# Optimization experiments

Hardware: AMD Instinct MI355X
Metric: run time of the kernel (lower is better)

The kernel has to match this reference:

```python
import jax, jax.numpy as jnp
import numpy as np


def _grouped_attn(q, k, v, mask, scale):
    # q: [T,H,D], k/v: [S,KH,D], mask: [T,S] or [KH,T,S] (True = visible)
    T, H, D = q.shape
    S, KH, _ = k.shape
    G = H // KH
    qg = q.reshape(T, KH, G, D)
    logits = jnp.einsum('tkgd,skd->kgts', qg, k) * scale
    if mask.ndim == 2:
        mask = jnp.broadcast_to(mask[None], (KH, T, S))
    logits = jnp.where(mask[:, None], logits, -1e30)
    p = jax.nn.softmax(logits, axis=-1)
    valid = mask.any(-1)  # [KH,T]: queries with at least one visible key
    p = jnp.where(valid[:, None, :, None], p, 0.0)
    o = jnp.einsum('kgts,skd->tkgd', p, v).reshape(T, H, D)
    return o, p


def setup_inputs() -> dict:
    key = jax.random.key(0)
    ks = jax.random.split(key, 4)
    T, H, KH, D = 2048, 16, 2, 128
    q = jax.random.normal(ks[0], (T, H, D), jnp.float32)
    k = jax.random.normal(ks[1], (T, KH, D), jnp.float32)
    v = jax.random.normal(ks[2], (T, KH, D), jnp.float32)
    w = jax.random.uniform(ks[3], (T, H, 3), jnp.float32)
    return dict(q=q, k=k, v=v, w=w, kernel_size=32, stride=16, block_size=64,
                top_n=16, num_init_blocks=1, num_local_blocks=2, window_size=512)


def reference(q, k, v, w, kernel_size, stride, block_size, top_n,
              num_init_blocks, num_local_blocks, window_size):
    T, H, D = q.shape
    KH = k.shape[1]
    scale = 1.0 / np.sqrt(D).astype(np.float32)
    t = jnp.arange(T)
    causal = t[None, :] <= t[:, None]  # [T,S]

    # ---- 1) compression: mean-pool overlapping windows of kernel_size / stride ----
    n_cmp = (T - kernel_size) // stride + 1
    starts = np.arange(n_cmp) * stride
    win_idx = starts[:, None] + np.arange(kernel_size)[None, :]  # [Ncmp,ks]
    cmp_k = k[win_idx].mean(axis=1)  # [Ncmp,KH,D]
    cmp_v = v[win_idx].mean(axis=1)
    j_end = jnp.asarray(starts) + kernel_size - 1
    cmp_mask = j_end[None, :] <= t[:, None]  # block fully in the past
    o_cmp, p_cmp = _grouped_attn(q, cmp_k, cmp_v, cmp_mask, scale)  # p_cmp [KH,G,T,Ncmp]

    # ---- 2) block selection from compressed attention probabilities ----
    n_blk = (T + block_size - 1) // block_size
    js, je = starts, starts + kernel_size
    bs_, be_ = np.arange(n_blk) * block_size, (np.arange(n_blk) + 1) * block_size
    M = jnp.asarray(((js[:, None] < be_[None, :]) & (bs_[None, :] < je[:, None])),
                    dtype=q.dtype)  # [Ncmp,Nblk] overlap indicator
    blk_score = jnp.einsum('kgtj,jb->ktb', p_cmp, M)  # sum over group heads

    b = jnp.arange(n_blk)
    t_blk = t // block_size
    forced = (b[None, :] < num_init_blocks) | \
             ((b[None, :] <= t_blk[:, None]) & (b[None, :] >= t_blk[:, None] - num_local_blocks + 1))
    blk_valid = (b[None, :] * block_size) <= t[:, None]
    score = jnp.where(forced[None], 1e30, blk_score)
    score = jnp.where(blk_valid[None], score, -1e30)
    _, idx = jax.lax.top_k(score, top_n)  # [KH,T,top_n]
    sel_blk = jax.nn.one_hot(idx, n_blk, dtype=q.dtype).sum(-2) > 0  # [KH,T,Nblk]

    # ---- 3) selected-block attention ----
    tok_sel = sel_blk[:, :, t // block_size]  # [KH,T,T]
    slc_mask = tok_sel & causal[None]
    o_slc, _ = _grouped_attn(q, k, v, slc_mask, scale)

    # ---- 4) sliding-window attention ----
    win_mask = causal & ((t[:, None] - t[None, :]) < window_size)
    o_win, _ = _grouped_attn(q, k, v, win_mask, scale)

    # ---- 5) gated combination ----
    o = w[..., 0:1] * o_cmp + w[..., 1:2] * o_slc + w[..., 2:3] * o_win
    return o
```

## Files before the change

kernel.cpp:

```cpp
#include <hip/hip_runtime.h>
#include <hip/hip_bf16.h>
#include <math.h>

#define T_ 2048
#define H_ 16
#define KH_ 2
#define G_ 8
#define D_ 128
#define NCMP 127
#define JP 128
#define NBLK 32
#define TOPN 16
#define WIN_ 512
#define SCALE 0.08838834764831845f

typedef __attribute__((ext_vector_type(8))) short short8;
typedef __attribute__((ext_vector_type(16))) float f32x16;

__device__ __forceinline__ unsigned short f2bf(float x) {
    union { float f; unsigned u; } c; c.f = x;
    unsigned u = c.u + 0x7fffu + ((c.u >> 16) & 1u);
    return (unsigned short)(u >> 16);
}
__device__ __forceinline__ float bf2f(unsigned short b) {
    union { unsigned u; float f; } c; c.u = (unsigned)b << 16; return c.f;
}

#define GLD16(gsrc, lds) \
    __builtin_amdgcn_global_load_lds( \
        (const __attribute__((address_space(1))) unsigned int*)(gsrc), \
        (__attribute__((address_space(3))) unsigned int*)(lds), 16, 0, 0)

__global__ __launch_bounds__(256) void prep_kv(
        const float* __restrict__ k, const float* __restrict__ v,
        unsigned short* __restrict__ kimg, unsigned short* __restrict__ vtimg) {
    const int b  = blockIdx.x;
    const int kh = blockIdx.y;
    const int s0 = b << 6;
    const int tid = threadIdx.x;
    const size_t tb = ((size_t)kh * 32 + b) * 8192;
#pragma unroll
    for (int it = 0; it < 4; ++it) {
        int idx = it * 256 + tid;
        int r = idx >> 4, c = idx & 15;
        const float* src = k + (size_t)(s0 + r) * (KH_ * D_) + kh * D_ + c * 8;
        float4 x = *reinterpret_cast<const float4*>(src);
        float4 y = *reinterpret_cast<const float4*>(src + 4);
        union { unsigned short u[8]; uint4 q; } o;
        o.u[0] = f2bf(x.x); o.u[1] = f2bf(x.y); o.u[2] = f2bf(x.z); o.u[3] = f2bf(x.w);
        o.u[4] = f2bf(y.x); o.u[5] = f2bf(y.y); o.u[6] = f2bf(y.z); o.u[7] = f2bf(y.w);
        *reinterpret_cast<uint4*>(&kimg[tb + r * 128 + ((c ^ ((r >> 2) & 7)) << 3)]) = o.q;
    }
#pragma unroll
    for (int it = 0; it < 4; ++it) {
        int idx = it * 256 + tid;
        int d = idx & 127, kc8 = idx >> 7;
        union { unsigned short u[8]; uint4 q; } o;
#pragma unroll
        for (int e = 0; e < 8; ++e)
            o.u[e] = f2bf(v[(size_t)(s0 + kc8 * 8 + e) * (KH_ * D_) + kh * D_ + d]);
        *reinterpret_cast<uint4*>(&vtimg[tb + d * 64 + ((kc8 ^ ((d >> 2) & 7)) << 3)]) = o.q;
    }
}

__global__ __launch_bounds__(128) void build_cmp(
        const float* __restrict__ k, const float* __restrict__ v,
        unsigned short* __restrict__ khiI, unsigned short* __restrict__ kloI,
        unsigned short* __restrict__ vflat) {
    int j  = blockIdx.x;
    int kh = blockIdx.y;
    int d  = threadIdx.x;
    unsigned short hb = 0, lb = 0, vb = 0;
    if (j < NCMP) {
        int s0 = j * 16;
        float sk = 0.f, sv = 0.f;
        for (int i = 0; i < 32; ++i) {
            sk += k[(size_t)(s0 + i) * KH_ * D_ + kh * D_ + d];
            sv += v[(size_t)(s0 + i) * KH_ * D_ + kh * D_ + d];
        }
        float mk = sk * (1.f / 32.f), mv = sv * (1.f / 32.f);
        hb = f2bf(mk);
        lb = f2bf(mk - bf2f(hb));
        vb = f2bf(mv);
    }
    int c = d >> 3;
    size_t ib = (size_t)kh * 16384 + j * 128 + ((c ^ ((j >> 2) & 7)) << 3) + (d & 7);
    khiI[ib] = hb;
    kloI[ib] = lb;
    vflat[(size_t)kh * 16384 + j * 128 + d] = vb;
}

__global__ __launch_bounds__(256) void prep_cmp_img(
        const unsigned short* __restrict__ vflat, unsigned short* __restrict__ cvtI) {
    const int kh = blockIdx.x;
    const int tid = threadIdx.x;
#pragma unroll
    for (int it = 0; it < 8; ++it) {
        int idx = it * 256 + tid;
        int d = idx & 127, jc8 = idx >> 7;
        union { unsigned short u[8]; uint4 q; } o;
#pragma unroll
        for (int e = 0; e < 8; ++e)
            o.u[e] = vflat[(size_t)kh * 16384 + (jc8 * 8 + e) * 128 + d];
        *reinterpret_cast<uint4*>(
            &cvtI[(size_t)kh * 16384 + d * 128 + ((jc8 ^ ((d >> 2) & 7)) << 3)]) = o.q;
    }
}

__global__ __launch_bounds__(256, 1) void cmp_attn_mfma(
        const float* __restrict__ q, const float* __restrict__ w,
        const unsigned short* __restrict__ khiI, const unsigned short* __restrict__ kloI,
        const unsigned short* __restrict__ cvtI,
        float* __restrict__ out, unsigned int* __restrict__ sel) {
    const int qt  = blockIdx.x;
    const int kh  = blockIdx.y;
    const int t0  = qt * 16;
    const int tid = threadIdx.x;
    const int wv  = tid >> 6;
    const int lane = tid & 63;
    const int l31 = lane & 31;
    const int hi  = lane >> 5;
    const int hi4 = hi * 4;

    __shared__ unsigned short KHI[JP * D_];
    __shared__ unsigned short KLO[JP * D_];
    __shared__ unsigned short CVT[JP * D_];
    __shared__ float wsc_s[16 * 132];
    __shared__ float bsc_s[16 * 32];
    __shared__ unsigned int sel_s[16];
    __shared__ float wfac[4][32];

    if (tid < 16) sel_s[tid] = 0u;
    for (int i = tid; i < 16 * 132; i += 256) wsc_s[i] = 0.f;

    const size_t cb = (size_t)kh * 16384;
#pragma unroll
    for (int it = 0; it < 8; ++it) {
        int off = (wv * 8 + it) * 512;
        GLD16(khiI + cb + off + lane * 8, &KHI[off]);
        GLD16(kloI + cb + off + lane * 8, &KLO[off]);
        GLD16(cvtI + cb + off + lane * 8, &CVT[off]);
    }

    const int qloc = l31 & 15;
    const int t    = t0 + qloc;
    const int h    = kh * G_ + 2 * wv + (l31 >> 4);
    short8 qhi[8], qlo[8];
    {
        const float* qrow = q + (size_t)t * (H_ * D_) + h * D_;
#pragma unroll
        for (int dc = 0; dc < 8; ++dc) {
            int d0 = dc * 16 + hi * 8;
            float4 x = *reinterpret_cast<const float4*>(qrow + d0);
            float4 y = *reinterpret_cast<const float4*>(qrow + d0 + 4);
            float e_[8] = {x.x, x.y, x.z, x.w, y.x, y.y, y.z, y.w};
            short8 fh, fl;
#pragma unroll
            for (int e = 0; e < 8; ++e) {
                unsigned short hb = f2bf(e_[e]);
                fh[e] = (short)hb;
                fl[e] = (short)f2bf(e_[e] - bf2f(hb));
            }
            qhi[dc] = fh; qlo[dc] = fl;
        }
    }
    __syncthreads();

    f32x16 s_[4];
#pragma unroll
    for (int tl = 0; tl < 4; ++tl)
#pragma unroll
        for (int r = 0; r < 16; ++r) s_[tl][r] = 0.f;
#pragma unroll
    for (int dc = 0; dc < 8; ++dc) {
        int c8 = dc * 2 + hi;
#pragma unroll
        for (int tl = 0; tl < 4; ++tl) {
            int row = tl * 32 + l31;
            int off = row * 128 + ((c8 ^ ((row >> 2) & 7)) << 3);
            short8 ahi = *reinterpret_cast<const short8*>(&KHI[off]);
            short8 alo = *reinterpret_cast<const short8*>(&KLO[off]);
            s_[tl] = __builtin_amdgcn_mfma_f32_32x32x16_bf16(ahi, qhi[dc], s_[tl], 0, 0, 0);
            s_[tl] = __builtin_amdgcn_mfma_f32_32x32x16_bf16(alo, qhi[dc], s_[tl], 0, 0, 0);
            s_[tl] = __builtin_amdgcn_mfma_f32_32x32x16_bf16(ahi, qlo[dc], s_[tl], 0, 0, 0);
        }
    }

    const int nv = (t >= 31) ? (((t - 31) >> 4) + 1) : 0;
    float m = -1e30f;
#pragma unroll
    for (int tl = 0; tl < 4; ++tl)
#pragma unroll
        for (int r = 0; r < 16; ++r) {
            int j = tl * 32 + (r & 3) + 8 * (r >> 2) + hi4;
            float lg = (j < nv) ? s_[tl][r] * SCALE : -1e30f;
            s_[tl][r] = lg;
            m = fmaxf(m, lg);
        }
    m = fmaxf(m, __shfl_xor(m, 32));
    float lsum = 0.f;
#pragma unroll
    for (int tl = 0; tl < 4; ++tl)
#pragma unroll
        for (int r = 0; r < 16; ++r) {
            float e = __expf(s_[tl][r] - m);
            s_[tl][r] = e;
            lsum += e;
        }
    lsum += __shfl_xor(lsum, 32);
    const float linv = (nv > 0) ? 1.f / lsum : 0.f;

#pragma unroll
    for (int tl = 0; tl < 4; ++tl)
#pragma unroll
        for (int r = 0; r < 16; ++r) {
            int j = tl * 32 + (r & 3) + 8 * (r >> 2) + hi4;
            atomicAdd(&wsc_s[qloc * 132 + j], s_[tl][r] * linv);
        }

    f32x16 acc[4];
#pragma unroll
    for (int dt = 0; dt < 4; ++dt)
#pragma unroll
        for (int r = 0; r < 16; ++r) acc[dt][r] = 0.f;
#pragma unroll
    for (int kc = 0; kc < 8; ++kc) {
        const int su = kc >> 1, rb = (kc & 1) * 8;
        unsigned pa0, pa1, pb0, pb1;
        asm("v_cvt_pk_bf16_f32 %0, %1, %2" : "=v"(pa0) : "v"(s_[su][rb+0]), "v"(s_[su][rb+1]));
        asm("v_cvt_pk_bf16_f32 %0, %1, %2" : "=v"(pa1) : "v"(s_[su][rb+2]), "v"(s_[su][rb+3]));
        asm("v_cvt_pk_bf16_f32 %0, %1, %2" : "=v"(pb0) : "v"(s_[su][rb+4]), "v"(s_[su][rb+5]));
        asm("v_cvt_pk_bf16_f32 %0, %1, %2" : "=v"(pb1) : "v"(s_[su][rb+6]), "v"(s_[su][rb+7]));
        unsigned sa0 = __shfl_xor(pa0, 32);
        unsigned sa1 = __shfl_xor(pa1, 32);
        unsigned sb0 = __shfl_xor(pb0, 32);
        unsigned sb1 = __shfl_xor(pb1, 32);
        union { unsigned u[4]; short8 s8; } pa;
        pa.u[0] = hi ? sb0 : pa0;
        pa.u[1] = hi ? sb1 : pa1;
        pa.u[2] = hi ? pb0 : sa0;
        pa.u[3] = hi ? pb1 : sa1;
        const int jc8 = kc * 2 + hi;
#pragma unroll
        for (int dt = 0; dt < 4; ++dt) {
            int d = dt * 32 + l31;
            short8 bf = *reinterpret_cast<const short8*>(
                &CVT[d * 128 + ((jc8 ^ ((d >> 2) & 7)) << 3)]);
            acc[dt] = __builtin_amdgcn_mfma_f32_32x32x16_bf16(pa.s8, bf, acc[dt], 0, 0, 0);
        }
    }

    wfac[wv][l31] = w[(size_t)t * (H_ * 3) + h * 3 + 0] * linv;
    __syncthreads();

    float wfr[16];
#pragma unroll
    for (int r = 0; r < 16; ++r)
        wfr[r] = wfac[wv][(r & 3) + 8 * (r >> 2) + hi4];
#pragma unroll
    for (int dt = 0; dt < 4; ++dt)
#pragma unroll
        for (int r = 0; r < 16; ++r) {
            int crow = (r & 3) + 8 * (r >> 2) + hi4;
            int tt = t0 + (crow & 15);
            int hh = kh * G_ + 2 * wv + (crow >> 4);
            out[(size_t)tt * (H_ * D_) + hh * D_ + dt * 32 + l31] = acc[dt][r] * wfr[r];
        }

#pragma unroll
    for (int half = 0; half < 2; ++half) {
        int b  = (tid & 15) + half * 16;
        int qq = tid >> 4;
        int tt = t0 + qq;
        float sc = 0.f;
        int j0 = 4 * b - 1; if (j0 < 0) j0 = 0;
        int j1 = 4 * b + 3; if (j1 > NCMP - 1) j1 = NCMP - 1;
        for (int j = j0; j <= j1; ++j) sc += wsc_s[qq * 132 + j];
        int tb = tt >> 6;
        bool forced = (b == 0) || (b <= tb && b >= tb - 1);
        if (forced) sc = 1e30f;
        if (b * 64 > tt) sc = -1e30f;
        bsc_s[qq * 32 + b] = sc;
    }
    __syncthreads();

#pragma unroll
    for (int half = 0; half < 2; ++half) {
        int b  = (tid & 15) + half * 16;
        int qq = tid >> 4;
        float sb = bsc_s[qq * 32 + b];
        int cnt = 0;
        for (int b2 = 0; b2 < NBLK; ++b2) {
            float s2 = bsc_s[qq * 32 + b2];
            cnt += (s2 > sb) || (s2 == sb && b2 < b);
        }
        if (cnt < TOPN) atomicOr(&sel_s[qq], 1u << b);
    }
    __syncthreads();
    if (tid < 16) sel[kh * T_ + t0 + tid] = sel_s[tid];
}

__global__ __launch_bounds__(256, 2) void slc_win_mfma(
        const float* __restrict__ q, const unsigned short* __restrict__ kimg,
        const unsigned short* __restrict__ vtimg, const float* __restrict__ w,
        const unsigned int* __restrict__ sel, float* __restrict__ out,
        float* __restrict__ winb, float* __restrict__ slcb, int use_scratch) {
    const int qt    = blockIdx.x;
    const int kh    = blockIdx.y;
    const int phase = blockIdx.z;
    const int t0    = qt * 16;
    const int tid   = threadIdx.x;
    const int wv    = tid >> 6;
    const int lane  = tid & 63;
    const int l31   = lane & 31;
    const int hi    = lane >> 5;
    const int hi4   = hi * 4;

    __shared__ unsigned short Kl[64 * 128];
    __shared__ unsigned short Vt[128 * 64];
    __shared__ float wfac[4][32];

    const int qloc = l31 & 15;
    const int t    = t0 + qloc;
    const int h    = kh * G_ + 2 * wv + (l31 >> 4);

    short8 qf[8];
    {
        const float* qrow = q + (size_t)t * (H_ * D_) + h * D_;
#pragma unroll
        for (int dc = 0; dc < 8; ++dc) {
            int d0 = dc * 16 + hi * 8;
            float4 x = *reinterpret_cast<const float4*>(qrow + d0);
            float4 y = *reinterpret_cast<const float4*>(qrow + d0 + 4);
            short8 f;
            f[0] = (short)f2bf(x.x); f[1] = (short)f2bf(x.y);
            f[2] = (short)f2bf(x.z); f[3] = (short)f2bf(x.w);
            f[4] = (short)f2bf(y.x); f[5] = (short)f2bf(y.y);
            f[6] = (short)f2bf(y.z); f[7] = (short)f2bf(y.w);
            qf[dc] = f;
        }
    }

    const unsigned int smask = sel[kh * T_ + t];
    const int tbmax = t0 >> 6;
    unsigned int um = 0;
    int b0 = 0;
    if (phase == 0) {
        int lo = t0 - (WIN_ - 1); if (lo < 0) lo = 0;
        b0 = lo >> 6;
    } else {
        unsigned int vm = (tbmax >= 31) ? 0xffffffffu : ((2u << tbmax) - 1u);
        um = smask;
        um |= __shfl_xor(um, 1); um |= __shfl_xor(um, 2);
        um |= __shfl_xor(um, 4); um |= __shfl_xor(um, 8);
        um &= vm;
    }

    f32x16 acc[4];
#pragma unroll
    for (int dt = 0; dt < 4; ++dt)
#pragma unroll
        for (int r = 0; r < 16; ++r) acc[dt][r] = 0.f;
    float m_run = -1e30f, l_run = 0.f;

    int bidx = b0;
    unsigned int rem = um;
    while (true) {
        int b;
        if (phase == 0) { if (bidx > tbmax) break; b = bidx++; }
        else            { if (!rem) break; b = __ffs(rem) - 1; rem &= rem - 1; }
        const int s0 = b << 6;

        __syncthreads();
        {
            const size_t tb = ((size_t)kh * 32 + b) * 8192;
#pragma unroll
            for (int it = 0; it < 4; ++it) {
                int off = (wv * 4 + it) * 512;
                GLD16(kimg + tb + off + lane * 8, &Kl[off]);
                GLD16(vtimg + tb + off + lane * 8, &Vt[off]);
            }
        }
        __syncthreads();

        f32x16 s_[2];
#pragma unroll
        for (int r = 0; r < 16; ++r) { s_[0][r] = 0.f; s_[1][r] = 0.f; }
#pragma unroll
        for (int dc = 0; dc < 8; ++dc) {
            int c8 = dc * 2 + hi;
            int swz = (c8 ^ ((l31 >> 2) & 7)) << 3;
            short8 a0 = *reinterpret_cast<const short8*>(&Kl[l31 * 128 + swz]);
            short8 a1 = *reinterpret_cast<const short8*>(&Kl[(32 + l31) * 128 + swz]);
            s_[0] = __builtin_amdgcn_mfma_f32_32x32x16_bf16(a0, qf[dc], s_[0], 0, 0, 0);
            s_[1] = __builtin_amdgcn_mfma_f32_32x32x16_bf16(a1, qf[dc], s_[1], 0, 0, 0);
        }

        const int sb = (smask >> b) & 1;
        float p_[2][16];
        float mc = -INFINITY;
#pragma unroll
        for (int sub = 0; sub < 2; ++sub)
#pragma unroll
            for (int r = 0; r < 16; ++r) {
                int crow = (r & 3) + 8 * (r >> 2) + hi4;
                int s = s0 + sub * 32 + crow;
                bool ok = (s <= t) && (phase ? (sb != 0) : (s + WIN_ > t));
                float lg = ok ? s_[sub][r] * SCALE : -INFINITY;
                p_[sub][r] = lg;
                mc = fmaxf(mc, lg);
            }
        mc = fmaxf(mc, __shfl_xor(mc, 1));
        mc = fmaxf(mc, __shfl_xor(mc, 2));
        mc = fmaxf(mc, __shfl_xor(mc, 4));
        mc = fmaxf(mc, __shfl_xor(mc, 8));
        mc = fmaxf(mc, __shfl_xor(mc, 16));
        mc = fmaxf(mc, __shfl_xor(mc, 32));
        float mnew = fmaxf(m_run, mc);
        float f = __expf(m_run - mnew);
        float lsum = 0.f;
#pragma unroll
        for (int sub = 0; sub < 2; ++sub)
#pragma unroll
            for (int r = 0; r < 16; ++r) {
                float e = __expf(p_[sub][r] - mnew);
                p_[sub][r] = e;
                lsum += e;
            }
        lsum += __shfl_xor(lsum, 32);
        l_run = l_run * f + lsum;
        m_run = mnew;
#pragma unroll
        for (int dt = 0; dt < 4; ++dt)
#pragma unroll
            for (int r = 0; r < 16; ++r) acc[dt][r] *= f;

#pragma unroll
        for (int kc = 0; kc < 4; ++kc) {
            const int su = kc >> 1, rb = (kc & 1) * 8;
            unsigned pa0, pb0, pa1, pb1;
            asm("v_cvt_pk_bf16_f32 %0, %1, %2" : "=v"(pa0) : "v"(p_[su][rb+0]), "v"(p_[su][rb+1]));
            asm("v_cvt_pk_bf16_f32 %0, %1, %2" : "=v"(pa1) : "v"(p_[su][rb+2]), "v"(p_[su][rb+3]));
            asm("v_cvt_pk_bf16_f32 %0, %1, %2" : "=v"(pb0) : "v"(p_[su][rb+4]), "v"(p_[su][rb+5]));
            asm("v_cvt_pk_bf16_f32 %0, %1, %2" : "=v"(pb1) : "v"(p_[su][rb+6]), "v"(p_[su][rb+7]));
            unsigned sa0 = __shfl_xor(pa0, 32);
            unsigned sa1 = __shfl_xor(pa1, 32);
            unsigned sb0 = __shfl_xor(pb0, 32);
            unsigned sb1 = __shfl_xor(pb1, 32);
            union { unsigned u[4]; short8 s8; } pa;
            pa.u[0] = hi ? sb0 : pa0;
            pa.u[1] = hi ? sb1 : pa1;
            pa.u[2] = hi ? pb0 : sa0;
            pa.u[3] = hi ? pb1 : sa1;
            const int kc8 = kc * 2 + hi;
#pragma unroll
            for (int dt = 0; dt < 4; ++dt) {
                int d = dt * 32 + l31;
                short8 bf = *reinterpret_cast<const short8*>(
                    &Vt[d * 64 + ((kc8 ^ ((d >> 2) & 7)) << 3)]);
                acc[dt] = __builtin_amdgcn_mfma_f32_32x32x16_bf16(pa.s8, bf, acc[dt], 0, 0, 0);
            }
        }
    }

    float linv = 1.f / l_run;
    int widx = (phase == 0) ? 2 : 1;
    wfac[wv][l31] = w[(size_t)t * (H_ * 3) + h * 3 + widx] * linv;
    __syncthreads();
    float wfr[16];
#pragma unroll
    for (int r = 0; r < 16; ++r)
        wfr[r] = wfac[wv][(r & 3) + 8 * (r >> 2) + hi4];
    float* base = (phase == 0) ? winb : slcb;
#pragma unroll
    for (int dt = 0; dt < 4; ++dt)
#pragma unroll
        for (int r = 0; r < 16; ++r) {
            int crow = (r & 3) + 8 * (r >> 2) + hi4;
            int tt = t0 + (crow & 15);
            int hh = kh * G_ + 2 * wv + (crow >> 4);
            size_t idx = (size_t)tt * (H_ * D_) + hh * D_ + dt * 32 + l31;
            float val = acc[dt][r] * wfr[r];
            if (use_scratch) base[idx] = val;
            else             atomicAdd(&out[idx], val);
        }
}

__global__ __launch_bounds__(256) void combine_out(float* __restrict__ out,
        const float* __restrict__ a, const float* __restrict__ b) {
    int i = blockIdx.x * 256 + threadIdx.x;
    float4 o = reinterpret_cast<float4*>(out)[i];
    float4 x = reinterpret_cast<const float4*>(a)[i];
    float4 y = reinterpret_cast<const float4*>(b)[i];
    o.x += x.x + y.x; o.y += x.y + y.y; o.z += x.z + y.z; o.w += x.w + y.w;
    reinterpret_cast<float4*>(out)[i] = o;
}

extern "C" void kernel_launch(void* const* d_in, const int* in_sizes, int n_in,
                              void* d_out, int out_size, void* d_ws, size_t ws_size,
                              hipStream_t stream) {
    const float* q = (const float*)d_in[0];
    const float* k = (const float*)d_in[1];
    const float* v = (const float*)d_in[2];
    const float* w = (const float*)d_in[3];
    float* out = (float*)d_out;

    char* ws = (char*)d_ws;
    unsigned short* kimg  = (unsigned short*)(ws);
    unsigned short* vtimg = (unsigned short*)(ws + (1u << 20));
    unsigned short* khiI  = (unsigned short*)(ws + (2u << 20));
    unsigned short* kloI  = (unsigned short*)(ws + (2u << 20) + 65536);
    unsigned short* cvtI  = (unsigned short*)(ws + (2u << 20) + 2 * 65536);
    unsigned short* vflat = (unsigned short*)(ws + (2u << 20) + 3 * 65536);
    unsigned int*   sel   = (unsigned int*)(ws + (2u << 20) + 4 * 65536);
    float* winb_s = (float*)(ws + (2u << 20) + 4 * 65536 + 16384);
    float* slcb_s = winb_s + (size_t)T_ * H_ * D_;
    const size_t need = (2u << 20) + 4 * 65536 + 16384
                        + 2 * (size_t)T_ * H_ * D_ * sizeof(float);
    const int use_scratch = (ws_size >= need) ? 1 : 0;
    float* winb = use_scratch ? winb_s : out;
    float* slcb = use_scratch ? slcb_s : out;

    hipLaunchKernelGGL(prep_kv, dim3(32, KH_), dim3(256), 0, stream, k, v, kimg, vtimg);
    hipLaunchKernelGGL(build_cmp, dim3(128, KH_), dim3(128), 0, stream,
                       k, v, khiI, kloI, vflat);
    hipLaunchKernelGGL(prep_cmp_img, dim3(KH_), dim3(256), 0, stream, vflat, cvtI);
    hipLaunchKernelGGL(cmp_attn_mfma, dim3(T_ / 16, KH_), dim3(256), 0, stream,
                       q, w, khiI, kloI, cvtI, out, sel);
    hipLaunchKernelGGL(slc_win_mfma, dim3(T_ / 16, KH_, 2), dim3(256), 0, stream,
                       q, kimg, vtimg, w, sel, out, winb, slcb, use_scratch);
    if (use_scratch) {
        hipLaunchKernelGGL(combine_out, dim3((T_ * H_ * D_ / 4) / 256), dim3(256), 0, stream,
                           out, winb, slcb);
    }
}
```

Before: 262.1 us.

## Double-buffer K/V tiles, change LDS swizzle, add setprio and reverse select-phase order

The sparse attention kernel now double-buffers its K and V LDS tiles. It prefetches the next selected block with async global-to-LDS loads while the MFMAs run on the current block, and it keeps one barrier per iteration instead of two. The LDS XOR swizzle moves from (row>>2)&7 to row&7 in every producer and consumer, aiming to cut bank conflicts on the 16-byte reads. MFMA sections are wrapped in s_setprio, and blocks in the selection phase run in reverse order to balance load against the windowed phase. The cost is doubled LDS for K and V, which may lower occupancy.

```diff
diff --git a/kernel.cpp b/kernel.cpp
--- a/kernel.cpp
+++ b/kernel.cpp
@@ -49,7 +49,7 @@
         union { unsigned short u[8]; uint4 q; } o;
         o.u[0] = f2bf(x.x); o.u[1] = f2bf(x.y); o.u[2] = f2bf(x.z); o.u[3] = f2bf(x.w);
         o.u[4] = f2bf(y.x); o.u[5] = f2bf(y.y); o.u[6] = f2bf(y.z); o.u[7] = f2bf(y.w);
-        *reinterpret_cast<uint4*>(&kimg[tb + r * 128 + ((c ^ ((r >> 2) & 7)) << 3)]) = o.q;
+        *reinterpret_cast<uint4*>(&kimg[tb + r * 128 + ((c ^ (r & 7)) << 3)]) = o.q;
     }
 #pragma unroll
     for (int it = 0; it < 4; ++it) {
@@ -59,7 +59,7 @@
 #pragma unroll
         for (int e = 0; e < 8; ++e)
             o.u[e] = f2bf(v[(size_t)(s0 + kc8 * 8 + e) * (KH_ * D_) + kh * D_ + d]);
-        *reinterpret_cast<uint4*>(&vtimg[tb + d * 64 + ((kc8 ^ ((d >> 2) & 7)) << 3)]) = o.q;
+        *reinterpret_cast<uint4*>(&vtimg[tb + d * 64 + ((kc8 ^ (d & 7)) << 3)]) = o.q;
     }
 }
 
@@ -84,7 +84,7 @@
         vb = f2bf(mv);
     }
     int c = d >> 3;
-    size_t ib = (size_t)kh * 16384 + j * 128 + ((c ^ ((j >> 2) & 7)) << 3) + (d & 7);
+    size_t ib = (size_t)kh * 16384 + j * 128 + ((c ^ (j & 7)) << 3) + (d & 7);
     khiI[ib] = hb;
     kloI[ib] = lb;
     vflat[(size_t)kh * 16384 + j * 128 + d] = vb;
@@ -103,7 +103,7 @@
         for (int e = 0; e < 8; ++e)
             o.u[e] = vflat[(size_t)kh * 16384 + (jc8 * 8 + e) * 128 + d];
         *reinterpret_cast<uint4*>(
-            &cvtI[(size_t)kh * 16384 + d * 128 + ((jc8 ^ ((d >> 2) & 7)) << 3)]) = o.q;
+            &cvtI[(size_t)kh * 16384 + d * 128 + ((jc8 ^ (d & 7)) << 3)]) = o.q;
     }
 }
 
@@ -171,13 +171,14 @@
     for (int tl = 0; tl < 4; ++tl)
 #pragma unroll
         for (int r = 0; r < 16; ++r) s_[tl][r] = 0.f;
+    __builtin_amdgcn_s_setprio(1);
 #pragma unroll
     for (int dc = 0; dc < 8; ++dc) {
         int c8 = dc * 2 + hi;
+        int swz = (c8 ^ (l31 & 7)) << 3;
 #pragma unroll
         for (int tl = 0; tl < 4; ++tl) {
-            int row = tl * 32 + l31;
-            int off = row * 128 + ((c8 ^ ((row >> 2) & 7)) << 3);
+            int off = (tl * 32 + l31) * 128 + swz;
             short8 ahi = *reinterpret_cast<const short8*>(&KHI[off]);
             short8 alo = *reinterpret_cast<const short8*>(&KLO[off]);
             s_[tl] = __builtin_amdgcn_mfma_f32_32x32x16_bf16(ahi, qhi[dc], s_[tl], 0, 0, 0);
@@ -185,6 +186,7 @@
             s_[tl] = __builtin_amdgcn_mfma_f32_32x32x16_bf16(ahi, qlo[dc], s_[tl], 0, 0, 0);
         }
     }
+    __builtin_amdgcn_s_setprio(0);
 
     const int nv = (t >= 31) ? (((t - 31) >> 4) + 1) : 0;
     float m = -1e30f;
@@ -241,13 +243,15 @@
         pa.u[2] = hi ? pb0 : sa0;
         pa.u[3] = hi ? pb1 : sa1;
         const int jc8 = kc * 2 + hi;
+        __builtin_amdgcn_s_setprio(1);
 #pragma unroll
         for (int dt = 0; dt < 4; ++dt) {
             int d = dt * 32 + l31;
             short8 bf = *reinterpret_cast<const short8*>(
-                &CVT[d * 128 + ((jc8 ^ ((d >> 2) & 7)) << 3)]);
+                &CVT[d * 128 + ((jc8 ^ (d & 7)) << 3)]);
             acc[dt] = __builtin_amdgcn_mfma_f32_32x32x16_bf16(pa.s8, bf, acc[dt], 0, 0, 0);
         }
+        __builtin_amdgcn_s_setprio(0);
     }
 
     wfac[wv][l31] = w[(size_t)t * (H_ * 3) + h * 3 + 0] * linv;
@@ -305,9 +309,9 @@
         const unsigned short* __restrict__ vtimg, const float* __restrict__ w,
         const unsigned int* __restrict__ sel, float* __restrict__ out,
         float* __restrict__ winb, float* __restrict__ slcb, int use_scratch) {
-    const int qt    = blockIdx.x;
+    const int phase = blockIdx.z;
+    const int qt    = phase ? (gridDim.x - 1 - blockIdx.x) : blockIdx.x;
     const int kh    = blockIdx.y;
-    const int phase = blockIdx.z;
     const int t0    = qt * 16;
     const int tid   = threadIdx.x;
     const int wv    = tid >> 6;
@@ -316,8 +320,8 @@
     const int hi    = lane >> 5;
     const int hi4   = hi * 4;
 
-    __shared__ unsigned short Kl[64 * 128];
-    __shared__ unsigned short Vt[128 * 64];
+    __shared__ unsigned short Kl[2][64 * 128];
+    __shared__ unsigned short Vt[2][128 * 64];
     __shared__ float wfac[4][32];
 
     const int qloc = l31 & 15;
@@ -343,17 +347,17 @@
 
     const unsigned int smask = sel[kh * T_ + t];
     const int tbmax = t0 >> 6;
-    unsigned int um = 0;
-    int b0 = 0;
+    unsigned int rem = 0;
+    int bidx = 0;
     if (phase == 0) {
         int lo = t0 - (WIN_ - 1); if (lo < 0) lo = 0;
-        b0 = lo >> 6;
+        bidx = lo >> 6;
     } else {
         unsigned int vm = (tbmax >= 31) ? 0xffffffffu : ((2u << tbmax) - 1u);
-        um = smask;
-        um |= __shfl_xor(um, 1); um |= __shfl_xor(um, 2);
-        um |= __shfl_xor(um, 4); um |= __shfl_xor(um, 8);
-        um &= vm;
+        rem = smask;
+        rem |= __shfl_xor(rem, 1); rem |= __shfl_xor(rem, 2);
+        rem |= __shfl_xor(rem, 4); rem |= __shfl_xor(rem, 8);
+        rem &= vm;
     }
 
     f32x16 acc[4];
@@ -363,40 +367,57 @@
         for (int r = 0; r < 16; ++r) acc[dt][r] = 0.f;
     float m_run = -1e30f, l_run = 0.f;
 
-    int bidx = b0;
-    unsigned int rem = um;
-    while (true) {
-        int b;
-        if (phase == 0) { if (bidx > tbmax) break; b = bidx++; }
-        else            { if (!rem) break; b = __ffs(rem) - 1; rem &= rem - 1; }
-        const int s0 = b << 6;
-
-        __syncthreads();
-        {
-            const size_t tb = ((size_t)kh * 32 + b) * 8192;
+    int b_cur;
+    if (phase == 0) b_cur = bidx++;
+    else { b_cur = rem ? (__ffs(rem) - 1) : -1; if (rem) rem &= rem - 1; }
+
+    if (b_cur >= 0) {
+        const size_t tb = ((size_t)kh * 32 + b_cur) * 8192;
+#pragma unroll
+        for (int it = 0; it < 4; ++it) {
+            int off = (wv * 4 + it) * 512;
+            GLD16(kimg + tb + off + lane * 8, &Kl[0][off]);
+            GLD16(vtimg + tb + off + lane * 8, &Vt[0][off]);
+        }
+    }
+    __syncthreads();
+
+    int cur = 0;
+    while (b_cur >= 0) {
+        int b_next;
+        if (phase == 0) b_next = (bidx <= tbmax) ? bidx++ : -1;
+        else { b_next = rem ? (__ffs(rem) - 1) : -1; if (rem) rem &= rem - 1; }
+
+        if (b_next >= 0) {
+            const size_t tb = ((size_t)kh * 32 + b_next) * 8192;
 #pragma unroll
             for (int it = 0; it < 4; ++it) {
                 int off = (wv * 4 + it) * 512;
-                GLD16(kimg + tb + off + lane * 8, &Kl[off]);
-                GLD16(vtimg + tb + off + lane * 8, &Vt[off]);
+                GLD16(kimg + tb + off + lane * 8, &Kl[cur ^ 1][off]);
+                GLD16(vtimg + tb + off + lane * 8, &Vt[cur ^ 1][off]);
             }
         }
-        __syncthreads();
+
+        const unsigned short* Kc = Kl[cur];
+        const unsigned short* Vc = Vt[cur];
+        const int s0 = b_cur << 6;
 
         f32x16 s_[2];
 #pragma unroll
         for (int r = 0; r < 16; ++r) { s_[0][r] = 0.f; s_[1][r] = 0.f; }
+        __builtin_amdgcn_s_setprio(1);
 #pragma unroll
         for (int dc = 0; dc < 8; ++dc) {
             int c8 = dc * 2 + hi;
-            int swz = (c8 ^ ((l31 >> 2) & 7)) << 3;
-            short8 a0 = *reinterpret_cast<const short8*>(&Kl[l31 * 128 + swz]);
-            short8 a1 = *reinterpret_cast<const short8*>(&Kl[(32 + l31) * 128 + swz]);
+            int swz = (c8 ^ (l31 & 7)) << 3;
+            short8 a0 = *reinterpret_cast<const short8*>(&Kc[l31 * 128 + swz]);
+            short8 a1 = *reinterpret_cast<const short8*>(&Kc[(32 + l31) * 128 + swz]);
             s_[0] = __builtin_amdgcn_mfma_f32_32x32x16_bf16(a0, qf[dc], s_[0], 0, 0, 0);
             s_[1] = __builtin_amdgcn_mfma_f32_32x32x16_bf16(a1, qf[dc], s_[1], 0, 0, 0);
         }
-
-        const int sb = (smask >> b) & 1;
+        __builtin_amdgcn_s_setprio(0);
+
+        const int sb = (smask >> b_cur) & 1;
         float p_[2][16];
         float mc = -INFINITY;
 #pragma unroll
@@ -453,14 +474,20 @@
             pa.u[2] = hi ? pb0 : sa0;
             pa.u[3] = hi ? pb1 : sa1;
             const int kc8 = kc * 2 + hi;
+            __builtin_amdgcn_s_setprio(1);
 #pragma unroll
             for (int dt = 0; dt < 4; ++dt) {
                 int d = dt * 32 + l31;
                 short8 bf = *reinterpret_cast<const short8*>(
-                    &Vt[d * 64 + ((kc8 ^ ((d >> 2) & 7)) << 3)]);
+                    &Vc[d * 64 + ((kc8 ^ (d & 7)) << 3)]);
                 acc[dt] = __builtin_amdgcn_mfma_f32_32x32x16_bf16(pa.s8, bf, acc[dt], 0, 0, 0);
             }
-        }
+            __builtin_amdgcn_s_setprio(0);
+        }
+
+        __syncthreads();
+        b_cur = b_next;
+        cur ^= 1;
     }
 
     float linv = 1.f / l_run;
```

New measurement: 258.7 us. About the same (-1.3%).
